# Performance work log

Hardware: AMD Instinct MI355X
Metric: run time of the kernel (lower is better)

The kernel has to match this reference:

```python
import jax, jax.numpy as jnp
import numpy as np

N_NODES = 100000
N_EDGES = 640000
D_FEAT = 128
UNITS = 128


def setup_inputs() -> dict:
    key = jax.random.key(0)
    k1, k2, k3, k4, k5 = jax.random.split(key, 5)
    X = jax.random.normal(k1, (N_NODES, D_FEAT), dtype=jnp.float32)
    ref_A = jax.random.randint(k2, (N_EDGES,), 0, N_NODES, dtype=jnp.int32)
    ref_B = jax.random.randint(k3, (N_EDGES,), 0, N_NODES, dtype=jnp.int32)
    # GlorotUniform-style params (scale approximated; exact init irrelevant for math)
    limit_w = np.sqrt(6.0 / (D_FEAT + UNITS)).astype(np.float32)
    w = jax.random.uniform(k4, (D_FEAT, UNITS), minval=-limit_w, maxval=limit_w, dtype=jnp.float32)
    b = jax.random.uniform(k5, (UNITS,), minval=-0.1, maxval=0.1, dtype=jnp.float32)
    return {"X": X, "ref_A": ref_A, "ref_B": ref_B, "w": w, "b": b}


def reference(X, ref_A, ref_B, w, b):
    # c.convolution: gather source-node features along edges, scatter-add to
    # destination nodes (sum aggregation over incoming messages).
    msgs = X[ref_A]                                        # [E, D]
    agg = jax.ops.segment_sum(msgs, ref_B, num_segments=X.shape[0])  # [N, D]
    out = agg @ w + b                                      # [N, units]
    return out
```

## Files before the change

kernel.cpp:

```cpp
#include <hip/hip_runtime.h>
#include <hip/hip_bf16.h>

typedef short s16x8 __attribute__((ext_vector_type(8)));
typedef float f32x4 __attribute__((ext_vector_type(4)));

#define CAPN 32

static __device__ inline unsigned short f2bf(float f) {
    __hip_bfloat16 h = __float2bfloat16(f);
    return *reinterpret_cast<unsigned short*>(&h);
}

__global__ __launch_bounds__(256) void fill_wt_kernel(
    const float* __restrict__ w, const int* __restrict__ A,
    const int* __restrict__ B, unsigned short* __restrict__ wT,
    int* __restrict__ cnt, unsigned int* __restrict__ entries, int E)
{
    int i = blockIdx.x * 256 + threadIdx.x;
    if (i < 16384) {
        int n = i >> 7, k = i & 127;
        wT[i] = f2bf(w[k * 128 + n]);
    }
    if (i < E) {
        int d = B[i];
        int pos = atomicAdd(&cnt[d], 1);
        if (pos < CAPN)
            entries[(size_t)d * CAPN + pos] = (unsigned int)A[i];
    }
}

__global__ __launch_bounds__(1024) void aggemm_kernel(
    const float* __restrict__ X, const int* __restrict__ cnt,
    const unsigned int* __restrict__ entries, const unsigned short* __restrict__ wT,
    const float* __restrict__ b, float* __restrict__ out, int N)
{
    __shared__ unsigned short atile[64 * 136];

    const int tid  = threadIdx.x;
    const int u    = tid >> 6;
    const int lane = tid & 63;
    const int m    = lane & 15;
    const int q    = lane >> 4;
    const int row0 = blockIdx.x * 64;
    const int nodeBase = row0 + u * 4;

    int deg[4];
    {
        int4 d4 = ((const int4*)cnt)[(row0 >> 2) + u];
        deg[0] = d4.x; deg[1] = d4.y; deg[2] = d4.z; deg[3] = d4.w;
    }
    int idxl[4];
    #pragma unroll
    for (int t = 0; t < 4; ++t) {
        int node = nodeBase + t;
        int dg = (node < N) ? min(deg[t], CAPN) : 0;
        deg[t] = dg;
        idxl[t] = (lane < dg) ? (int)entries[(size_t)node * CAPN + lane] : 0;
    }

    #pragma unroll
    for (int t = 0; t < 4; ++t) {
        const int dg = deg[t];
        float ax = 0.f, ay = 0.f;
        const int chunks = (dg + 7) >> 3;
        #pragma unroll 1
        for (int ch = 0; ch < chunks; ++ch) {
            const int base = ch * 8;
            float2 p[8];
            #pragma unroll
            for (int j = 0; j < 8; ++j) {
                int sl = base + j;
                if (sl > dg - 1) sl = dg - 1;
                int s = __shfl(idxl[t], sl);
                p[j] = *(const float2*)(X + (size_t)s * 128 + lane * 2);
            }
            #pragma unroll
            for (int j = 0; j < 8; ++j)
                if (base + j < dg) { ax += p[j].x; ay += p[j].y; }
        }
        ((unsigned int*)atile)[(u * 4 + t) * 68 + lane] =
            (unsigned int)f2bf(ax) | ((unsigned int)f2bf(ay) << 16);
    }
    __syncthreads();

    if (u < 4) {
        const unsigned short* arow = &atile[(u * 16 + m) * 136];
        f32x4 acc[8] = {};
        #pragma unroll
        for (int s = 0; s < 4; ++s) {
            s16x8 a = *(const s16x8*)&arow[s * 32 + q * 8];
            #pragma unroll
            for (int c = 0; c < 8; ++c) {
                s16x8 bf = *(const s16x8*)&wT[(size_t)(c * 16 + m) * 128 + s * 32 + q * 8];
                acc[c] = __builtin_amdgcn_mfma_f32_16x16x32_bf16(a, bf, acc[c], 0, 0, 0);
            }
        }
        const int r0g = row0 + u * 16 + q * 4;
        #pragma unroll
        for (int c = 0; c < 8; ++c) {
            int col = c * 16 + m;
            float bias = b[col];
            #pragma unroll
            for (int r = 0; r < 4; ++r) {
                int row = r0g + r;
                if (row < N)
                    out[(size_t)row * 128 + col] = acc[c][r] + bias;
            }
        }
    }
}

extern "C" void kernel_launch(void* const* d_in, const int* in_sizes, int n_in,
                              void* d_out, int out_size, void* d_ws, size_t ws_size,
                              hipStream_t stream) {
    const float* X = (const float*)d_in[0];
    const int*   A = (const int*)d_in[1];
    const int*   B = (const int*)d_in[2];
    const float* w = (const float*)d_in[3];
    const float* b = (const float*)d_in[4];
    float* out = (float*)d_out;

    const int N = in_sizes[0] / 128;
    const int E = in_sizes[1];

    char* wsb = (char*)d_ws;
    size_t off = 0;
    int* cnt = (int*)(wsb + off); off += (size_t)4 * N;
    off = (off + 255) & ~(size_t)255;
    unsigned short* wT = (unsigned short*)(wsb + off); off += 32768;
    unsigned int* entries = (unsigned int*)(wsb + off);

    hipMemsetAsync(cnt, 0, (size_t)4 * N, stream);
    fill_wt_kernel<<<(E + 255) / 256, 256, 0, stream>>>(w, A, B, wT, cnt, entries, E);
    aggemm_kernel<<<(N + 63) / 64, 1024, 0, stream>>>(X, cnt, entries, wT, b, out, N);
}
```

Measured before the change: 216.9 us.

## Gather from bf16 copy of X and interleave four nodes' gathers per wave

Adds a pre-pass in the fill kernel that converts X to bf16 in workspace, so the edge gather reads half the bytes per message. The aggregation loop now runs over all four nodes of a wave together in each chunk, giving more independent loads in flight. This costs an extra full read of X plus a bf16 write, and rounds messages to bf16 before accumulation, which adds error. A fallback to the fp32 path is kept for when the workspace is too small.

New measurement: 212.3 us. 2.1% less time.

```diff
diff --git a/kernel.cpp b/kernel.cpp
--- a/kernel.cpp
+++ b/kernel.cpp
@@ -11,16 +11,28 @@
     return *reinterpret_cast<unsigned short*>(&h);
 }
 
-__global__ __launch_bounds__(256) void fill_wt_kernel(
+__global__ __launch_bounds__(256) void fill_kernel(
     const float* __restrict__ w, const int* __restrict__ A,
-    const int* __restrict__ B, unsigned short* __restrict__ wT,
-    int* __restrict__ cnt, unsigned int* __restrict__ entries, int E)
+    const int* __restrict__ B, const float* __restrict__ X,
+    unsigned short* __restrict__ wT, unsigned short* __restrict__ Xh,
+    int* __restrict__ cnt, unsigned int* __restrict__ entries,
+    int E, int total8, int doConv)
 {
     int i = blockIdx.x * 256 + threadIdx.x;
     if (i < 16384) {
         int n = i >> 7, k = i & 127;
         wT[i] = f2bf(w[k * 128 + n]);
     }
+    if (doConv && i < total8) {
+        const float4* xv = (const float4*)X + (size_t)i * 2;
+        float4 lo = xv[0], hi = xv[1];
+        union { unsigned short u[8]; uint4 v; } r;
+        r.u[0] = f2bf(lo.x); r.u[1] = f2bf(lo.y);
+        r.u[2] = f2bf(lo.z); r.u[3] = f2bf(lo.w);
+        r.u[4] = f2bf(hi.x); r.u[5] = f2bf(hi.y);
+        r.u[6] = f2bf(hi.z); r.u[7] = f2bf(hi.w);
+        ((uint4*)Xh)[i] = r.v;
+    }
     if (i < E) {
         int d = B[i];
         int pos = atomicAdd(&cnt[d], 1);
@@ -29,10 +41,12 @@
     }
 }
 
+template<int BF>
 __global__ __launch_bounds__(1024) void aggemm_kernel(
-    const float* __restrict__ X, const int* __restrict__ cnt,
-    const unsigned int* __restrict__ entries, const unsigned short* __restrict__ wT,
-    const float* __restrict__ b, float* __restrict__ out, int N)
+    const float* __restrict__ X, const unsigned short* __restrict__ Xh,
+    const int* __restrict__ cnt, const unsigned int* __restrict__ entries,
+    const unsigned short* __restrict__ wT, const float* __restrict__ b,
+    float* __restrict__ out, int N)
 {
     __shared__ unsigned short atile[64 * 136];
 
@@ -58,28 +72,66 @@
         idxl[t] = (lane < dg) ? (int)entries[(size_t)node * CAPN + lane] : 0;
     }
 
-    #pragma unroll
-    for (int t = 0; t < 4; ++t) {
-        const int dg = deg[t];
-        float ax = 0.f, ay = 0.f;
-        const int chunks = (dg + 7) >> 3;
+    if constexpr (BF) {
+        int last[4];
+        #pragma unroll
+        for (int t = 0; t < 4; ++t) last[t] = (deg[t] > 0) ? deg[t] - 1 : 0;
+        const int maxdg = max(max(deg[0], deg[1]), max(deg[2], deg[3]));
+        const int maxch = (maxdg + 7) >> 3;
+        float ax[4] = {0.f, 0.f, 0.f, 0.f};
+        float ay[4] = {0.f, 0.f, 0.f, 0.f};
         #pragma unroll 1
-        for (int ch = 0; ch < chunks; ++ch) {
+        for (int ch = 0; ch < maxch; ++ch) {
             const int base = ch * 8;
-            float2 p[8];
-            #pragma unroll
-            for (int j = 0; j < 8; ++j) {
-                int sl = base + j;
-                if (sl > dg - 1) sl = dg - 1;
-                int s = __shfl(idxl[t], sl);
-                p[j] = *(const float2*)(X + (size_t)s * 128 + lane * 2);
-            }
-            #pragma unroll
-            for (int j = 0; j < 8; ++j)
-                if (base + j < dg) { ax += p[j].x; ay += p[j].y; }
-        }
-        ((unsigned int*)atile)[(u * 4 + t) * 68 + lane] =
-            (unsigned int)f2bf(ax) | ((unsigned int)f2bf(ay) << 16);
+            unsigned int p[4][8];
+            #pragma unroll
+            for (int t = 0; t < 4; ++t) {
+                #pragma unroll
+                for (int j = 0; j < 8; ++j) {
+                    int sl = base + j;
+                    if (sl > last[t]) sl = last[t];
+                    int s = __shfl(idxl[t], sl);
+                    p[t][j] = *(const unsigned int*)(Xh + (size_t)s * 128 + lane * 2);
+                }
+            }
+            #pragma unroll
+            for (int t = 0; t < 4; ++t) {
+                #pragma unroll
+                for (int j = 0; j < 8; ++j)
+                    if (base + j < deg[t]) {
+                        ax[t] += __uint_as_float(p[t][j] << 16);
+                        ay[t] += __uint_as_float(p[t][j] & 0xFFFF0000u);
+                    }
+            }
+        }
+        #pragma unroll
+        for (int t = 0; t < 4; ++t)
+            ((unsigned int*)atile)[(u * 4 + t) * 68 + lane] =
+                (unsigned int)f2bf(ax[t]) | ((unsigned int)f2bf(ay[t]) << 16);
+    } else {
+        #pragma unroll
+        for (int t = 0; t < 4; ++t) {
+            const int dg = deg[t];
+            float ax = 0.f, ay = 0.f;
+            const int chunks = (dg + 7) >> 3;
+            #pragma unroll 1
+            for (int ch = 0; ch < chunks; ++ch) {
+                const int base = ch * 8;
+                float2 p[8];
+                #pragma unroll
+                for (int j = 0; j < 8; ++j) {
+                    int sl = base + j;
+                    if (sl > dg - 1) sl = dg - 1;
+                    int s = __shfl(idxl[t], sl);
+                    p[j] = *(const float2*)(X + (size_t)s * 128 + lane * 2);
+                }
+                #pragma unroll
+                for (int j = 0; j < 8; ++j)
+                    if (base + j < dg) { ax += p[j].x; ay += p[j].y; }
+            }
+            ((unsigned int*)atile)[(u * 4 + t) * 68 + lane] =
+                (unsigned int)f2bf(ax) | ((unsigned int)f2bf(ay) << 16);
+        }
     }
     __syncthreads();
 
@@ -128,9 +180,21 @@
     int* cnt = (int*)(wsb + off); off += (size_t)4 * N;
     off = (off + 255) & ~(size_t)255;
     unsigned short* wT = (unsigned short*)(wsb + off); off += 32768;
-    unsigned int* entries = (unsigned int*)(wsb + off);
+    unsigned int* entries = (unsigned int*)(wsb + off); off += (size_t)N * CAPN * 4;
+    off = (off + 255) & ~(size_t)255;
+    unsigned short* Xh = (unsigned short*)(wsb + off);
+    const size_t need = off + (size_t)N * 128 * 2;
+    const int useBf = (ws_size >= need) ? 1 : 0;
 
     hipMemsetAsync(cnt, 0, (size_t)4 * N, stream);
-    fill_wt_kernel<<<(E + 255) / 256, 256, 0, stream>>>(w, A, B, wT, cnt, entries, E);
-    aggemm_kernel<<<(N + 63) / 64, 1024, 0, stream>>>(X, cnt, entries, wT, b, out, N);
-}
+    const int total8 = N * 16;
+    const int workItems = useBf ? (total8 > E ? total8 : E) : E;
+    fill_kernel<<<(workItems + 255) / 256, 256, 0, stream>>>(
+        w, A, B, X, wT, Xh, cnt, entries, E, total8, useBf);
+    if (useBf)
+        aggemm_kernel<1><<<(N + 63) / 64, 1024, 0, stream>>>(
+            X, Xh, cnt, entries, wT, b, out, N);
+    else
+        aggemm_kernel<0><<<(N + 63) / 64, 1024, 0, stream>>>(
+            X, Xh, cnt, entries, wT, b, out, N);
+}
```

## Apply weight before aggregation, gather bf16 projected rows, overlap CSR build with GEMM

Applied to the files above, without the earlier changes.

Reorders the computation to out = segment_sum((X@w)[A]) + b. It computes Y = X@w once per node using split-bf16 (hi/lo, three MFMAs) to keep fp32-like accuracy, stores Y as bf16, and then gathers and sums bf16 rows per destination. The CSR bucketing and the GEMM run as separate block ranges of one launch, and the memset is folded into the weight-prep kernel. This halves gather bytes per edge and removes the per-block GEMM after aggregation. In exchange it adds an N×128 bf16 intermediate write, three times the MFMA work, and bf16 rounding of the projected values before summation.

Result: slower. 237.2 us (+9.4%).

```diff
diff --git a/kernel.cpp b/kernel.cpp
--- a/kernel.cpp
+++ b/kernel.cpp
@@ -10,102 +10,158 @@
     __hip_bfloat16 h = __float2bfloat16(f);
     return *reinterpret_cast<unsigned short*>(&h);
 }
-
-__global__ __launch_bounds__(256) void fill_wt_kernel(
-    const float* __restrict__ w, const int* __restrict__ A,
-    const int* __restrict__ B, unsigned short* __restrict__ wT,
-    int* __restrict__ cnt, unsigned int* __restrict__ entries, int E)
+static __device__ inline float bf2f(unsigned short u) {
+    return __uint_as_float((unsigned int)u << 16);
+}
+
+__global__ __launch_bounds__(256) void zwt_kernel(
+    const float* __restrict__ w, unsigned short* __restrict__ wTh,
+    unsigned short* __restrict__ wTl, int* __restrict__ cnt, int Ncap)
 {
     int i = blockIdx.x * 256 + threadIdx.x;
+    if (i < Ncap) cnt[i] = 0;
     if (i < 16384) {
         int n = i >> 7, k = i & 127;
-        wT[i] = f2bf(w[k * 128 + n]);
-    }
-    if (i < E) {
-        int d = B[i];
-        int pos = atomicAdd(&cnt[d], 1);
-        if (pos < CAPN)
-            entries[(size_t)d * CAPN + pos] = (unsigned int)A[i];
-    }
-}
-
-__global__ __launch_bounds__(1024) void aggemm_kernel(
-    const float* __restrict__ X, const int* __restrict__ cnt,
-    const unsigned int* __restrict__ entries, const unsigned short* __restrict__ wT,
-    const float* __restrict__ b, float* __restrict__ out, int N)
+        float v = w[k * 128 + n];
+        unsigned short hi = f2bf(v);
+        wTh[i] = hi;
+        wTl[i] = f2bf(v - bf2f(hi));
+    }
+}
+
+__global__ __launch_bounds__(256, 6) void gb_kernel(
+    const float* __restrict__ X, const int* __restrict__ A,
+    const int* __restrict__ B, const unsigned short* __restrict__ wTh,
+    const unsigned short* __restrict__ wTl, int* __restrict__ cnt,
+    unsigned int* __restrict__ entries, unsigned short* __restrict__ Yh,
+    int N, int E, int EB)
 {
-    __shared__ unsigned short atile[64 * 136];
-
-    const int tid  = threadIdx.x;
+    const int tid = threadIdx.x;
+
+    if (blockIdx.x < EB) {
+        int i0 = blockIdx.x * 512 + tid * 2;
+        if (i0 + 1 < E) {
+            int2 a2 = *(const int2*)(A + i0);
+            int2 b2 = *(const int2*)(B + i0);
+            int p0 = atomicAdd(&cnt[b2.x], 1);
+            int p1 = atomicAdd(&cnt[b2.y], 1);
+            if (p0 < CAPN) entries[(size_t)b2.x * CAPN + p0] = (unsigned int)a2.x;
+            if (p1 < CAPN) entries[(size_t)b2.y * CAPN + p1] = (unsigned int)a2.y;
+        } else if (i0 < E) {
+            int a = A[i0], d = B[i0];
+            int p0 = atomicAdd(&cnt[d], 1);
+            if (p0 < CAPN) entries[(size_t)d * CAPN + p0] = (unsigned int)a;
+        }
+        return;
+    }
+
+    const int gbid = blockIdx.x - EB;
     const int u    = tid >> 6;
     const int lane = tid & 63;
     const int m    = lane & 15;
     const int q    = lane >> 4;
-    const int row0 = blockIdx.x * 64;
-    const int nodeBase = row0 + u * 4;
+    const int r0   = gbid * 64;
+    const int row  = r0 + u * 16 + m;
+    const int rldr = (row < N) ? row : (N - 1);
+
+    f32x4 acc[8] = {};
+    #pragma unroll
+    for (int s = 0; s < 4; ++s) {
+        const float* xr = X + (size_t)rldr * 128 + s * 32 + q * 8;
+        float4 x0 = *(const float4*)xr;
+        float4 x1 = *(const float4*)(xr + 4);
+        float xv[8] = {x0.x, x0.y, x0.z, x0.w, x1.x, x1.y, x1.z, x1.w};
+        s16x8 ahi, alo;
+        #pragma unroll
+        for (int j = 0; j < 8; ++j) {
+            unsigned short h = f2bf(xv[j]);
+            ahi[j] = (short)h;
+            alo[j] = (short)f2bf(xv[j] - bf2f(h));
+        }
+        #pragma unroll
+        for (int c = 0; c < 8; ++c) {
+            const size_t wo = (size_t)(c * 16 + m) * 128 + s * 32 + q * 8;
+            s16x8 bh = *(const s16x8*)&wTh[wo];
+            s16x8 bl = *(const s16x8*)&wTl[wo];
+            acc[c] = __builtin_amdgcn_mfma_f32_16x16x32_bf16(ahi, bh, acc[c], 0, 0, 0);
+            acc[c] = __builtin_amdgcn_mfma_f32_16x16x32_bf16(alo, bh, acc[c], 0, 0, 0);
+            acc[c] = __builtin_amdgcn_mfma_f32_16x16x32_bf16(ahi, bl, acc[c], 0, 0, 0);
+        }
+    }
+    const int r0g = r0 + u * 16 + q * 4;
+    #pragma unroll
+    for (int c = 0; c < 8; ++c) {
+        int col = c * 16 + m;
+        #pragma unroll
+        for (int r = 0; r < 4; ++r) {
+            int orow = r0g + r;
+            if (orow < N)
+                Yh[(size_t)orow * 128 + col] = f2bf(acc[c][r]);
+        }
+    }
+}
+
+__global__ __launch_bounds__(256, 6) void gather_kernel(
+    const int* __restrict__ cnt, const unsigned int* __restrict__ entries,
+    const unsigned short* __restrict__ Yh, const float* __restrict__ b,
+    float* __restrict__ out, int N)
+{
+    const int tid  = threadIdx.x;
+    const int u    = tid >> 6;
+    const int lane = tid & 63;
+    const int nodeBase = blockIdx.x * 16 + u * 4;
 
     int deg[4];
     {
-        int4 d4 = ((const int4*)cnt)[(row0 >> 2) + u];
+        int4 d4 = ((const int4*)cnt)[blockIdx.x * 4 + u];
         deg[0] = d4.x; deg[1] = d4.y; deg[2] = d4.z; deg[3] = d4.w;
     }
-    int idxl[4];
+    int idxl[4], last[4];
     #pragma unroll
     for (int t = 0; t < 4; ++t) {
         int node = nodeBase + t;
         int dg = (node < N) ? min(deg[t], CAPN) : 0;
         deg[t] = dg;
+        last[t] = (dg > 0) ? dg - 1 : 0;
         idxl[t] = (lane < dg) ? (int)entries[(size_t)node * CAPN + lane] : 0;
     }
 
-    #pragma unroll
-    for (int t = 0; t < 4; ++t) {
-        const int dg = deg[t];
-        float ax = 0.f, ay = 0.f;
-        const int chunks = (dg + 7) >> 3;
-        #pragma unroll 1
-        for (int ch = 0; ch < chunks; ++ch) {
-            const int base = ch * 8;
-            float2 p[8];
+    const int maxdg = max(max(deg[0], deg[1]), max(deg[2], deg[3]));
+    const int maxch = (maxdg + 7) >> 3;
+    float ax[4] = {0.f, 0.f, 0.f, 0.f};
+    float ay[4] = {0.f, 0.f, 0.f, 0.f};
+    #pragma unroll 1
+    for (int ch = 0; ch < maxch; ++ch) {
+        const int base = ch * 8;
+        unsigned int p[4][8];
+        #pragma unroll
+        for (int t = 0; t < 4; ++t) {
             #pragma unroll
             for (int j = 0; j < 8; ++j) {
                 int sl = base + j;
-                if (sl > dg - 1) sl = dg - 1;
+                if (sl > last[t]) sl = last[t];
                 int s = __shfl(idxl[t], sl);
-                p[j] = *(const float2*)(X + (size_t)s * 128 + lane * 2);
+                p[t][j] = *(const unsigned int*)(Yh + (size_t)s * 128 + lane * 2);
             }
+        }
+        #pragma unroll
+        for (int t = 0; t < 4; ++t) {
             #pragma unroll
             for (int j = 0; j < 8; ++j)
-                if (base + j < dg) { ax += p[j].x; ay += p[j].y; }
-        }
-        ((unsigned int*)atile)[(u * 4 + t) * 68 + lane] =
-            (unsigned int)f2bf(ax) | ((unsigned int)f2bf(ay) << 16);
-    }
-    __syncthreads();
-
-    if (u < 4) {
-        const unsigned short* arow = &atile[(u * 16 + m) * 136];
-        f32x4 acc[8] = {};
-        #pragma unroll
-        for (int s = 0; s < 4; ++s) {
-            s16x8 a = *(const s16x8*)&arow[s * 32 + q * 8];
-            #pragma unroll
-            for (int c = 0; c < 8; ++c) {
-                s16x8 bf = *(const s16x8*)&wT[(size_t)(c * 16 + m) * 128 + s * 32 + q * 8];
-                acc[c] = __builtin_amdgcn_mfma_f32_16x16x32_bf16(a, bf, acc[c], 0, 0, 0);
-            }
-        }
-        const int r0g = row0 + u * 16 + q * 4;
-        #pragma unroll
-        for (int c = 0; c < 8; ++c) {
-            int col = c * 16 + m;
-            float bias = b[col];
-            #pragma unroll
-            for (int r = 0; r < 4; ++r) {
-                int row = r0g + r;
-                if (row < N)
-                    out[(size_t)row * 128 + col] = acc[c][r] + bias;
-            }
+                if (base + j < deg[t]) {
+                    ax[t] += __uint_as_float(p[t][j] << 16);
+                    ay[t] += __uint_as_float(p[t][j] & 0xFFFF0000u);
+                }
+        }
+    }
+
+    const float2 bb = ((const float2*)b)[lane];
+    #pragma unroll
+    for (int t = 0; t < 4; ++t) {
+        int node = nodeBase + t;
+        if (node < N) {
+            float2 o = {ax[t] + bb.x, ay[t] + bb.y};
+            ((float2*)(out + (size_t)node * 128))[lane] = o;
         }
     }
 }
@@ -122,15 +178,24 @@
 
     const int N = in_sizes[0] / 128;
     const int E = in_sizes[1];
+    const int Ncap = (N + 15) & ~15;
 
     char* wsb = (char*)d_ws;
     size_t off = 0;
-    int* cnt = (int*)(wsb + off); off += (size_t)4 * N;
+    int* cnt = (int*)(wsb + off); off += (size_t)4 * Ncap;
     off = (off + 255) & ~(size_t)255;
-    unsigned short* wT = (unsigned short*)(wsb + off); off += 32768;
-    unsigned int* entries = (unsigned int*)(wsb + off);
-
-    hipMemsetAsync(cnt, 0, (size_t)4 * N, stream);
-    fill_wt_kernel<<<(E + 255) / 256, 256, 0, stream>>>(w, A, B, wT, cnt, entries, E);
-    aggemm_kernel<<<(N + 63) / 64, 1024, 0, stream>>>(X, cnt, entries, wT, b, out, N);
-}
+    unsigned short* wTh = (unsigned short*)(wsb + off); off += 32768;
+    unsigned short* wTl = (unsigned short*)(wsb + off); off += 32768;
+    unsigned int* entries = (unsigned int*)(wsb + off); off += (size_t)N * CAPN * 4;
+    off = (off + 255) & ~(size_t)255;
+    unsigned short* Yh = (unsigned short*)(wsb + off);
+
+    const int zItems = (Ncap > 16384) ? Ncap : 16384;
+    zwt_kernel<<<(zItems + 255) / 256, 256, 0, stream>>>(w, wTh, wTl, cnt, Ncap);
+
+    const int EB = (E + 511) / 512;
+    const int GB = (N + 63) / 64;
+    gb_kernel<<<EB + GB, 256, 0, stream>>>(X, A, B, wTh, wTl, cnt, entries, Yh, N, E, EB);
+
+    gather_kernel<<<(N + 15) / 16, 256, 0, stream>>>(cnt, entries, Yh, b, out, N);
+}
```
